# Kernel optimization log

Measured on AMD Instinct MI355X. Metric: run time of the kernel, lower is better.

## Reference

```python
import jax, jax.numpy as jnp
import numpy as np


def setup_inputs() -> dict:
    key = jax.random.key(0)
    k0, k1, k2, k3, k4 = jax.random.split(key, 5)
    dim, b, h, w = 256, 32, 56, 56
    x = jax.random.normal(k0, (b, dim, h, w), jnp.float32)
    # 1x1 conv qk: weight [out=dim, in=dim], bias [dim]
    qk_w = jax.random.normal(k1, (dim, dim), jnp.float32) * (1.0 / np.sqrt(dim))
    qk_b = jax.random.normal(k2, (dim,), jnp.float32) * 0.01
    # depthwise 3x3 conv pe: weight [dim, 1, 3, 3], bias [dim]
    pe_w = jax.random.normal(k3, (dim, 1, 3, 3), jnp.float32) * (1.0 / 3.0)
    pe_b = jax.random.normal(k4, (dim,), jnp.float32) * 0.01
    return {"x": x, "qk_w": qk_w, "qk_b": qk_b, "pe_w": pe_w, "pe_b": pe_b}


def reference(x, qk_w, qk_b, pe_w, pe_b):
    b, c, h, w = x.shape
    n = h * w
    d = c // 2                      # head_dim = dim // 2
    s = float(n) ** -0.5
    # 1x1 conv + (elu + 1) feature map
    qk = jnp.einsum('bchw,oc->bohw', x, qk_w) + qk_b[None, :, None, None]
    qk = jax.nn.elu(qk) + 1.0
    qk = qk.reshape(b, 2, d, n)
    q, k = qk[:, 0], qk[:, 1]       # each [b, d, n]
    v = x.reshape(b, c, n)          # [b, c, n]
    # kv outer product: (k*s) @ (v^T * s) -> [b, d, c]
    kv = jnp.einsum('bdn,bcn->bdc', k, v) * (s * s)
    # numerator q^T @ kv -> [b, n, c]
    num = jnp.einsum('bdn,bdc->bnc', q, kv)
    # denominator q^T @ mean(k, axis=-1) -> [b, n, 1]
    den = jnp.einsum('bdn,bd->bn', q, jnp.mean(k, axis=-1))[:, :, None] + 1e-6
    attn = (num / den).transpose(0, 2, 1).reshape(b, c, h, w)
    # depthwise 3x3 positional conv on v (= x)
    pe = jax.lax.conv_general_dilated(
        x, pe_w, window_strides=(1, 1), padding='SAME',
        dimension_numbers=('NCHW', 'OIHW', 'NCHW'), feature_group_count=c)
    return attn + pe + pe_b[None, :, None, None]
```

## Files before the change

kernel.cpp:

```cpp
#include <hip/hip_runtime.h>

#define B_ 32
#define C_ 256
#define D_ 128
#define HH 56
#define WW 56
#define N_ 3136
#define KSPLIT 14
#define KRANGE 224

typedef float f32x4 __attribute__((ext_vector_type(4)));
typedef short s16x8 __attribute__((ext_vector_type(8)));
typedef unsigned short u16x8 __attribute__((ext_vector_type(8)));

__device__ __forceinline__ int swz4(int r){
  return (r & 3) ^ (((r >> 2) & 1) << 1) ^ ((r >> 3) & 1);
}
__device__ __forceinline__ unsigned short f2bf(float f){
  unsigned u = __float_as_uint(f);
  u += 0x7fffu + ((u >> 16) & 1u);
  return (unsigned short)(u >> 16);
}
__device__ __forceinline__ float bf2f(unsigned short h){
  return __uint_as_float(((unsigned)h) << 16);
}
__device__ __forceinline__ float elu1(float v){
  return v > 0.f ? v + 1.f : __expf(v);
}

template<int R>
__device__ __forceinline__ void stage_glds(const unsigned short* gp, int ld, char* lds){
  const int tid = threadIdx.x;
  const int wid = tid >> 6;
#pragma unroll
  for (int q = 0; q < R/64; ++q){
    const int slot = q*256 + tid;
    const int r = slot >> 2, gi = slot & 3;
    const int u = gi ^ swz4(r);
    const unsigned short* ga = gp + r*ld + u*8;
    char* lb = lds + (q*256 + wid*64)*16;
    __builtin_amdgcn_global_load_lds(
        (__attribute__((address_space(1))) void*)ga,
        (__attribute__((address_space(3))) void*)lb, 16, 0, 0);
  }
}

__device__ __forceinline__ s16x8 ldsfrag(const char* lds, int r, int g){
  return *(const s16x8*)(lds + r*64 + ((g ^ swz4(r)) << 4));
}

__global__ __launch_bounds__(256) void k1_qk(
    const float* __restrict__ x, const float* __restrict__ w,
    const float* __restrict__ bias,
    unsigned short* __restrict__ kbuf, unsigned short* __restrict__ qt)
{
  __shared__ __align__(16) char Al[256*64];
  __shared__ __align__(16) char Bl[64*64];
  const int tid = threadIdx.x, lane = tid & 63, wid = tid >> 6;
  const int n0 = blockIdx.x * 64;
  const int b  = blockIdx.y;
  const float* xb = x + (size_t)b*C_*N_;
  const int wo = wid*64;
  f32x4 acc[4][4] = {};

  for (int k0 = 0; k0 < C_; k0 += 32){
    __syncthreads();
#pragma unroll
    for (int q = 0; q < 8; ++q){
      int idx = q*256 + tid;
      int r = idx >> 3, c4 = (idx & 7)*4;
      float4 v = *(const float4*)(w + (size_t)r*C_ + k0 + c4);
      ushort4 hv = {f2bf(v.x), f2bf(v.y), f2bf(v.z), f2bf(v.w)};
      *(ushort4*)(Al + r*64 + ((c4*2) ^ (swz4(r) << 4))) = hv;
    }
#pragma unroll
    for (int q = 0; q < 2; ++q){
      int idx = q*256 + tid;
      int cc = idx >> 4, nn = (idx & 15)*4;
      float4 v = *(const float4*)(xb + (size_t)(k0 + cc)*N_ + n0 + nn);
      float vv[4] = {v.x, v.y, v.z, v.w};
#pragma unroll
      for (int i = 0; i < 4; ++i){
        int r = nn + i;
        *(unsigned short*)(Bl + r*64 + ((cc*2) ^ (swz4(r) << 4))) = f2bf(vv[i]);
      }
    }
    __syncthreads();
    s16x8 af[4], bv4[4];
#pragma unroll
    for (int m = 0; m < 4; ++m)  af[m]  = ldsfrag(Al, wo + m*16 + (lane & 15), lane >> 4);
#pragma unroll
    for (int nf = 0; nf < 4; ++nf) bv4[nf] = ldsfrag(Bl, nf*16 + (lane & 15), lane >> 4);
#pragma unroll
    for (int m = 0; m < 4; ++m)
#pragma unroll
      for (int nf = 0; nf < 4; ++nf)
        acc[m][nf] = __builtin_amdgcn_mfma_f32_16x16x32_bf16(af[m], bv4[nf], acc[m][nf], 0, 0, 0);
  }

  const int col = lane & 15, rg = lane >> 4;
  if (wid < 2){
#pragma unroll
    for (int m = 0; m < 4; ++m){
      const int db = wo + m*16 + rg*4;
      const float b0 = bias[db], b1 = bias[db+1], b2 = bias[db+2], b3 = bias[db+3];
#pragma unroll
      for (int nf = 0; nf < 4; ++nf){
        const int n = n0 + nf*16 + col;
        f32x4 a = acc[m][nf];
        ushort4 hv = {f2bf(elu1(a[0]+b0)), f2bf(elu1(a[1]+b1)),
                      f2bf(elu1(a[2]+b2)), f2bf(elu1(a[3]+b3))};
        *(ushort4*)(qt + ((size_t)b*N_ + n)*D_ + db) = hv;
      }
    }
  } else {
#pragma unroll
    for (int m = 0; m < 4; ++m)
#pragma unroll
      for (int j = 0; j < 4; ++j){
        const int d = wo - 128 + m*16 + rg*4 + j;
        const float bb = bias[128 + d];
#pragma unroll
        for (int nf = 0; nf < 4; ++nf){
          const int n = n0 + nf*16 + col;
          kbuf[((size_t)b*D_ + d)*N_ + n] = f2bf(elu1(acc[m][nf][j] + bb));
        }
      }
  }
}

__global__ __launch_bounds__(256) void k2_kv(
    const unsigned short* __restrict__ kbuf, const float* __restrict__ x,
    unsigned short* __restrict__ kvp, float* __restrict__ kmp)
{
  __shared__ __align__(16) char Al[128*64];
  __shared__ __align__(16) char Bl[128*64];
  const int tid = threadIdx.x, lane = tid & 63, wid = tid >> 6;
  const int c0 = blockIdx.x * 128;
  const int ks = blockIdx.y;
  const int b  = blockIdx.z;
  const unsigned short* kb = kbuf + (size_t)b*D_*N_ + ks*KRANGE;
  const float* xb = x + ((size_t)b*C_ + c0)*N_ + ks*KRANGE;
  const int wd = (wid >> 1)*64, wc = (wid & 1)*64;
  f32x4 acc[4][4] = {};
  float kms = 0.f;
  const bool do_km = (c0 == 0);

  for (int t = 0; t < KRANGE/32; ++t){
    __syncthreads();
    stage_glds<128>(kb + t*32, N_, Al);
#pragma unroll
    for (int q = 0; q < 4; ++q){
      int idx = q*256 + tid;
      int cc = idx >> 3, n4 = (idx & 7)*4;
      float4 v = *(const float4*)(xb + (size_t)cc*N_ + t*32 + n4);
      ushort4 hv = {f2bf(v.x), f2bf(v.y), f2bf(v.z), f2bf(v.w)};
      *(ushort4*)(Bl + cc*64 + ((n4*2) ^ (swz4(cc) << 4))) = hv;
    }
    __syncthreads();
    s16x8 af[4], bv4[4];
#pragma unroll
    for (int m = 0; m < 4; ++m)  af[m]  = ldsfrag(Al, wd + m*16 + (lane & 15), lane >> 4);
#pragma unroll
    for (int cf = 0; cf < 4; ++cf) bv4[cf] = ldsfrag(Bl, wc + cf*16 + (lane & 15), lane >> 4);
#pragma unroll
    for (int m = 0; m < 4; ++m)
#pragma unroll
      for (int cf = 0; cf < 4; ++cf)
        acc[m][cf] = __builtin_amdgcn_mfma_f32_16x16x32_bf16(af[m], bv4[cf], acc[m][cf], 0, 0, 0);
    if (do_km){
      const int dr = tid >> 1, half = tid & 1;
      const char* base = Al + dr*64;
      const int s = swz4(dr);
      uint4 u0 = *(const uint4*)(base + (((half*2 + 0) ^ s) << 4));
      uint4 u1 = *(const uint4*)(base + (((half*2 + 1) ^ s) << 4));
      const unsigned ua[8] = {u0.x,u0.y,u0.z,u0.w,u1.x,u1.y,u1.z,u1.w};
#pragma unroll
      for (int i = 0; i < 8; ++i){
        kms += bf2f((unsigned short)(ua[i] & 0xffffu));
        kms += bf2f((unsigned short)(ua[i] >> 16));
      }
    }
  }

  if (do_km){
    kms += __shfl_xor(kms, 1);
    if ((tid & 1) == 0) kmp[((size_t)b*KSPLIT + ks)*D_ + (tid >> 1)] = kms;
  }
  const int col = lane & 15, rg = lane >> 4;
#pragma unroll
  for (int m = 0; m < 4; ++m)
#pragma unroll
    for (int j = 0; j < 4; ++j){
      const int d = wd + m*16 + rg*4 + j;
#pragma unroll
      for (int cf = 0; cf < 4; ++cf){
        const int c = c0 + wc + cf*16 + col;
        kvp[(((size_t)b*KSPLIT + ks)*D_ + d)*C_ + c] = f2bf(acc[m][cf][j]);
      }
    }
}

__global__ __launch_bounds__(256) void kr_reduce(
    const unsigned short* __restrict__ kvp, const float* __restrict__ kmp,
    unsigned short* __restrict__ kvt, float* __restrict__ km)
{
  __shared__ float T[64][65];
  const int tid = threadIdx.x;
  const int ct = blockIdx.x, dt = blockIdx.y, b = blockIdx.z;
  const int d0 = dt*64, c0 = ct*64;
  const int r = tid >> 2, cq = (tid & 3)*16;
  float v[16] = {};
  for (int j = 0; j < KSPLIT; ++j){
    const unsigned short* p = kvp + (((size_t)b*KSPLIT + j)*D_ + d0 + r)*C_ + c0 + cq;
#pragma unroll
    for (int i = 0; i < 16; ++i) v[i] += bf2f(p[i]);
  }
  const float sc = 1.0f/(float)N_;
#pragma unroll
  for (int i = 0; i < 16; ++i) T[r][cq + i] = v[i]*sc;
  __syncthreads();
  u16x8 h0, h1;
#pragma unroll
  for (int i = 0; i < 8; ++i) h0[i] = f2bf(T[cq + i][r]);
#pragma unroll
  for (int i = 0; i < 8; ++i) h1[i] = f2bf(T[cq + 8 + i][r]);
  unsigned short* o = kvt + ((size_t)b*C_ + c0 + r)*D_ + d0 + cq;
  *(u16x8*)o = h0;
  *(u16x8*)(o + 8) = h1;
  if (ct == 0 && dt == 0 && tid < D_){
    float s = 0.f;
    for (int j = 0; j < KSPLIT; ++j) s += kmp[((size_t)b*KSPLIT + j)*D_ + tid];
    km[b*D_ + tid] = s*sc;
  }
}

__global__ __launch_bounds__(256) void k3_attn(
    const unsigned short* __restrict__ qt, const unsigned short* __restrict__ kvt,
    const float* __restrict__ km, unsigned short* __restrict__ attn)
{
  __shared__ __align__(16) char SM[128*72*2];
  char* Al = SM;
  char* Bl = SM + 128*64;
  unsigned short* P = (unsigned short*)SM;
  __shared__ float kms[128];
  __shared__ float dens[64];
  const int tid = threadIdx.x, lane = tid & 63, wid = tid >> 6;
  const int n0 = blockIdx.x * 64;
  const int c0 = blockIdx.y * 128;
  const int b  = blockIdx.z;
  if (tid < 128) kms[tid] = km[b*D_ + tid];
  const unsigned short* kvb = kvt + ((size_t)b*C_ + c0)*D_;
  const unsigned short* qtb = qt + ((size_t)b*N_ + n0)*D_;
  const int wc = (wid >> 1)*64, wn = (wid & 1)*32;
  f32x4 acc[4][2] = {};
  float den = 0.f;

  for (int k0 = 0; k0 < D_; k0 += 32){
    __syncthreads();
    stage_glds<128>(kvb + k0, D_, Al);
    stage_glds<64>(qtb + k0, D_, Bl);
    __syncthreads();
    s16x8 af[4], bv4[2];
#pragma unroll
    for (int m = 0; m < 4; ++m)  af[m]  = ldsfrag(Al, wc + m*16 + (lane & 15), lane >> 4);
#pragma unroll
    for (int nf = 0; nf < 2; ++nf) bv4[nf] = ldsfrag(Bl, wn + nf*16 + (lane & 15), lane >> 4);
#pragma unroll
    for (int m = 0; m < 4; ++m)
#pragma unroll
      for (int nf = 0; nf < 2; ++nf)
        acc[m][nf] = __builtin_amdgcn_mfma_f32_16x16x32_bf16(af[m], bv4[nf], acc[m][nf], 0, 0, 0);
    {
      const int nr = tid >> 2, g = tid & 3;
      uint4 u = *(const uint4*)(Bl + nr*64 + ((g ^ swz4(nr)) << 4));
      const float* kp = kms + k0 + g*8;
      const unsigned ua[4] = {u.x, u.y, u.z, u.w};
#pragma unroll
      for (int i = 0; i < 4; ++i){
        den += bf2f((unsigned short)(ua[i] & 0xffffu)) * kp[i*2];
        den += bf2f((unsigned short)(ua[i] >> 16))     * kp[i*2 + 1];
      }
    }
  }
  den += __shfl_xor(den, 1);
  den += __shfl_xor(den, 2);
  if ((tid & 3) == 0) dens[tid >> 2] = den;
  __syncthreads();

  const int col = lane & 15, rg = lane >> 4;
  float rdv[2];
#pragma unroll
  for (int nf = 0; nf < 2; ++nf)
    rdv[nf] = 1.0f / (dens[wn + nf*16 + col] + 1e-6f);
#pragma unroll
  for (int m = 0; m < 4; ++m)
#pragma unroll
    for (int nf = 0; nf < 2; ++nf)
#pragma unroll
      for (int j = 0; j < 4; ++j)
        P[(wc + m*16 + rg*4 + j)*72 + (wn + nf*16 + col)] = f2bf(acc[m][nf][j] * rdv[nf]);
  __syncthreads();

#pragma unroll
  for (int p = 0; p < 4; ++p){
    const int c = (tid >> 3) + p*32, ch = tid & 7;
    u16x8 v = *(const u16x8*)(P + c*72 + ch*8);
    *(u16x8*)(attn + ((size_t)b*C_ + c0 + c)*N_ + n0 + ch*8) = v;
  }
}

__global__ __launch_bounds__(256) void k4_pe(
    const float* __restrict__ x, const unsigned short* __restrict__ attn,
    const float* __restrict__ pw, const float* __restrict__ pb,
    float* __restrict__ out)
{
  __shared__ float xs[N_];
  const int ch = blockIdx.x, b = blockIdx.y;
  const float* xp = x + ((size_t)b*C_ + ch)*N_;
  for (int i = threadIdx.x; i < N_/4; i += 256)
    ((float4*)xs)[i] = ((const float4*)xp)[i];
  const float* wp = pw + ch*9;
  const float w00=wp[0], w01=wp[1], w02=wp[2];
  const float w10=wp[3], w11=wp[4], w12=wp[5];
  const float w20=wp[6], w21=wp[7], w22=wp[8];
  const float bias = pb[ch];
  __syncthreads();
  const unsigned short* ap = attn + ((size_t)b*C_ + ch)*N_;
  float* op = out + ((size_t)b*C_ + ch)*N_;
  for (int i = threadIdx.x; i < N_; i += 256) {
    const int hh = i / WW, ww = i - hh*WW;
    float s = bias;
    if (hh > 0) {
      const float* rp = &xs[(hh-1)*WW];
      if (ww > 0)      s += w00 * rp[ww-1];
                       s += w01 * rp[ww];
      if (ww < WW-1)   s += w02 * rp[ww+1];
    }
    {
      const float* rp = &xs[hh*WW];
      if (ww > 0)      s += w10 * rp[ww-1];
                       s += w11 * rp[ww];
      if (ww < WW-1)   s += w12 * rp[ww+1];
    }
    if (hh < HH-1) {
      const float* rp = &xs[(hh+1)*WW];
      if (ww > 0)      s += w20 * rp[ww-1];
                       s += w21 * rp[ww];
      if (ww < WW-1)   s += w22 * rp[ww+1];
    }
    op[i] = bf2f(ap[i]) + s;
  }
}

extern "C" void kernel_launch(void* const* d_in, const int* in_sizes, int n_in,
                              void* d_out, int out_size, void* d_ws, size_t ws_size,
                              hipStream_t stream) {
  (void)in_sizes; (void)n_in; (void)out_size; (void)ws_size;
  const float* x   = (const float*)d_in[0];
  const float* qkw = (const float*)d_in[1];
  const float* qkb = (const float*)d_in[2];
  const float* pew = (const float*)d_in[3];
  const float* peb = (const float*)d_in[4];
  float* out = (float*)d_out;

  unsigned short* kbuf = (unsigned short*)d_ws;
  unsigned short* qt   = kbuf + (size_t)B_*D_*N_;
  unsigned short* kvt  = qt   + (size_t)B_*N_*D_;
  float* km  = (float*)(kvt + (size_t)B_*C_*D_);
  unsigned short* kvp  = (unsigned short*)(km + (size_t)B_*D_);
  float* kmp = (float*)(kvp + (size_t)B_*KSPLIT*D_*C_);
  unsigned short* attn = kvp;

  k1_qk    <<<dim3(N_/64, B_),         256, 0, stream>>>(x, qkw, qkb, kbuf, qt);
  k2_kv    <<<dim3(C_/128, KSPLIT, B_),256, 0, stream>>>(kbuf, x, kvp, kmp);
  kr_reduce<<<dim3(4, 2, B_),          256, 0, stream>>>(kvp, kmp, kvt, km);
  k3_attn  <<<dim3(N_/64, 2, B_),      256, 0, stream>>>(qt, kvt, km, attn);
  k4_pe    <<<dim3(C_, B_),            256, 0, stream>>>(x, attn, pew, peb, out);
}
```

Before: 181.0 us.

## Pre-transpose x and weights to bf16, use async LDS loads, widen kv tile

Adds pre-pass kernels that convert the qk weight to bf16 and transpose x into an [b,n,c] bf16 layout. k1 can then stage both operands with direct global-to-LDS loads instead of doing per-element conversion and scattered LDS stores. k2 now covers all 256 channels per block, so k is loaded once rather than twice, and the k-sum runs in every block. Hardware packed bf16 conversion replaces the manual rounding in several places. The cost is an extra full pass over x (read fp32, write bf16), more workspace aliasing, and twice the accumulator registers in k2.

New measurement: 186.7 us. +3.1%, slower.

```diff
diff --git a/kernel.cpp b/kernel.cpp
--- a/kernel.cpp
+++ b/kernel.cpp
@@ -26,6 +26,11 @@
 }
 __device__ __forceinline__ float elu1(float v){
   return v > 0.f ? v + 1.f : __expf(v);
+}
+__device__ __forceinline__ unsigned cvtpk(float lo, float hi){
+  unsigned r;
+  asm("v_cvt_pk_bf16_f32 %0, %1, %2" : "=v"(r) : "v"(lo), "v"(hi));
+  return r;
 }
 
 template<int R>
@@ -49,8 +54,41 @@
   return *(const s16x8*)(lds + r*64 + ((g ^ swz4(r)) << 4));
 }
 
+__global__ __launch_bounds__(256) void k0_w(
+    const float* __restrict__ w, unsigned short* __restrict__ wb)
+{
+  const int i = blockIdx.x*256 + threadIdx.x;
+  float4 v = *(const float4*)(w + (size_t)i*4);
+  uint2 h = {cvtpk(v.x, v.y), cvtpk(v.z, v.w)};
+  *(uint2*)(wb + (size_t)i*4) = h;
+}
+
+__global__ __launch_bounds__(256) void k0_t(
+    const float* __restrict__ x, unsigned short* __restrict__ xt)
+{
+  __shared__ float T[64][65];
+  const int tid = threadIdx.x;
+  const int n0 = blockIdx.x*64, c0 = blockIdx.y*64, b = blockIdx.z;
+  const float* xb = x + ((size_t)b*C_ + c0)*N_ + n0;
+#pragma unroll
+  for (int q = 0; q < 4; ++q){
+    const int cr = q*16 + (tid >> 4), nc = (tid & 15)*4;
+    float4 v = *(const float4*)(xb + (size_t)cr*N_ + nc);
+    T[cr][nc+0] = v.x; T[cr][nc+1] = v.y; T[cr][nc+2] = v.z; T[cr][nc+3] = v.w;
+  }
+  __syncthreads();
+  const int nn = tid >> 2, cq = tid & 3;
+  unsigned h[8];
+#pragma unroll
+  for (int j = 0; j < 8; ++j)
+    h[j] = cvtpk(T[cq*16 + 2*j][nn], T[cq*16 + 2*j + 1][nn]);
+  unsigned short* dst = xt + ((size_t)b*N_ + n0 + nn)*C_ + c0 + cq*16;
+  *(uint4*)dst       = (uint4){h[0], h[1], h[2], h[3]};
+  *(uint4*)(dst + 8) = (uint4){h[4], h[5], h[6], h[7]};
+}
+
 __global__ __launch_bounds__(256) void k1_qk(
-    const float* __restrict__ x, const float* __restrict__ w,
+    const unsigned short* __restrict__ xt, const unsigned short* __restrict__ wb,
     const float* __restrict__ bias,
     unsigned short* __restrict__ kbuf, unsigned short* __restrict__ qt)
 {
@@ -59,32 +97,14 @@
   const int tid = threadIdx.x, lane = tid & 63, wid = tid >> 6;
   const int n0 = blockIdx.x * 64;
   const int b  = blockIdx.y;
-  const float* xb = x + (size_t)b*C_*N_;
+  const unsigned short* xtb = xt + ((size_t)b*N_ + n0)*C_;
   const int wo = wid*64;
   f32x4 acc[4][4] = {};
 
   for (int k0 = 0; k0 < C_; k0 += 32){
     __syncthreads();
-#pragma unroll
-    for (int q = 0; q < 8; ++q){
-      int idx = q*256 + tid;
-      int r = idx >> 3, c4 = (idx & 7)*4;
-      float4 v = *(const float4*)(w + (size_t)r*C_ + k0 + c4);
-      ushort4 hv = {f2bf(v.x), f2bf(v.y), f2bf(v.z), f2bf(v.w)};
-      *(ushort4*)(Al + r*64 + ((c4*2) ^ (swz4(r) << 4))) = hv;
-    }
-#pragma unroll
-    for (int q = 0; q < 2; ++q){
-      int idx = q*256 + tid;
-      int cc = idx >> 4, nn = (idx & 15)*4;
-      float4 v = *(const float4*)(xb + (size_t)(k0 + cc)*N_ + n0 + nn);
-      float vv[4] = {v.x, v.y, v.z, v.w};
-#pragma unroll
-      for (int i = 0; i < 4; ++i){
-        int r = nn + i;
-        *(unsigned short*)(Bl + r*64 + ((cc*2) ^ (swz4(r) << 4))) = f2bf(vv[i]);
-      }
-    }
+    stage_glds<256>(wb + k0, C_, Al);
+    stage_glds<64>(xtb + k0, C_, Bl);
     __syncthreads();
     s16x8 af[4], bv4[4];
 #pragma unroll
@@ -108,9 +128,9 @@
       for (int nf = 0; nf < 4; ++nf){
         const int n = n0 + nf*16 + col;
         f32x4 a = acc[m][nf];
-        ushort4 hv = {f2bf(elu1(a[0]+b0)), f2bf(elu1(a[1]+b1)),
-                      f2bf(elu1(a[2]+b2)), f2bf(elu1(a[3]+b3))};
-        *(ushort4*)(qt + ((size_t)b*N_ + n)*D_ + db) = hv;
+        uint2 hv = {cvtpk(elu1(a[0]+b0), elu1(a[1]+b1)),
+                    cvtpk(elu1(a[2]+b2), elu1(a[3]+b3))};
+        *(uint2*)(qt + ((size_t)b*N_ + n)*D_ + db) = hv;
       }
     }
   } else {
@@ -134,41 +154,39 @@
     unsigned short* __restrict__ kvp, float* __restrict__ kmp)
 {
   __shared__ __align__(16) char Al[128*64];
-  __shared__ __align__(16) char Bl[128*64];
+  __shared__ __align__(16) char Bl[256*64];
   const int tid = threadIdx.x, lane = tid & 63, wid = tid >> 6;
-  const int c0 = blockIdx.x * 128;
-  const int ks = blockIdx.y;
-  const int b  = blockIdx.z;
+  const int ks = blockIdx.x;
+  const int b  = blockIdx.y;
   const unsigned short* kb = kbuf + (size_t)b*D_*N_ + ks*KRANGE;
-  const float* xb = x + ((size_t)b*C_ + c0)*N_ + ks*KRANGE;
-  const int wd = (wid >> 1)*64, wc = (wid & 1)*64;
-  f32x4 acc[4][4] = {};
+  const float* xb = x + (size_t)b*C_*N_ + ks*KRANGE;
+  const int wd = (wid >> 1)*64, wc = (wid & 1)*128;
+  f32x4 acc[4][8] = {};
   float kms = 0.f;
-  const bool do_km = (c0 == 0);
 
   for (int t = 0; t < KRANGE/32; ++t){
     __syncthreads();
     stage_glds<128>(kb + t*32, N_, Al);
 #pragma unroll
-    for (int q = 0; q < 4; ++q){
+    for (int q = 0; q < 8; ++q){
       int idx = q*256 + tid;
       int cc = idx >> 3, n4 = (idx & 7)*4;
       float4 v = *(const float4*)(xb + (size_t)cc*N_ + t*32 + n4);
-      ushort4 hv = {f2bf(v.x), f2bf(v.y), f2bf(v.z), f2bf(v.w)};
-      *(ushort4*)(Bl + cc*64 + ((n4*2) ^ (swz4(cc) << 4))) = hv;
-    }
-    __syncthreads();
-    s16x8 af[4], bv4[4];
-#pragma unroll
-    for (int m = 0; m < 4; ++m)  af[m]  = ldsfrag(Al, wd + m*16 + (lane & 15), lane >> 4);
-#pragma unroll
-    for (int cf = 0; cf < 4; ++cf) bv4[cf] = ldsfrag(Bl, wc + cf*16 + (lane & 15), lane >> 4);
+      uint2 h = {cvtpk(v.x, v.y), cvtpk(v.z, v.w)};
+      *(uint2*)(Bl + cc*64 + ((n4*2) ^ (swz4(cc) << 4))) = h;
+    }
+    __syncthreads();
+    s16x8 af[4], bv[8];
+#pragma unroll
+    for (int m = 0; m < 4; ++m)  af[m] = ldsfrag(Al, wd + m*16 + (lane & 15), lane >> 4);
+#pragma unroll
+    for (int cf = 0; cf < 8; ++cf) bv[cf] = ldsfrag(Bl, wc + cf*16 + (lane & 15), lane >> 4);
 #pragma unroll
     for (int m = 0; m < 4; ++m)
 #pragma unroll
-      for (int cf = 0; cf < 4; ++cf)
-        acc[m][cf] = __builtin_amdgcn_mfma_f32_16x16x32_bf16(af[m], bv4[cf], acc[m][cf], 0, 0, 0);
-    if (do_km){
+      for (int cf = 0; cf < 8; ++cf)
+        acc[m][cf] = __builtin_amdgcn_mfma_f32_16x16x32_bf16(af[m], bv[cf], acc[m][cf], 0, 0, 0);
+    {
       const int dr = tid >> 1, half = tid & 1;
       const char* base = Al + dr*64;
       const int s = swz4(dr);
@@ -183,10 +201,9 @@
     }
   }
 
-  if (do_km){
-    kms += __shfl_xor(kms, 1);
-    if ((tid & 1) == 0) kmp[((size_t)b*KSPLIT + ks)*D_ + (tid >> 1)] = kms;
-  }
+  kms += __shfl_xor(kms, 1);
+  if ((tid & 1) == 0) kmp[((size_t)b*KSPLIT + ks)*D_ + (tid >> 1)] = kms;
+
   const int col = lane & 15, rg = lane >> 4;
 #pragma unroll
   for (int m = 0; m < 4; ++m)
@@ -194,8 +211,8 @@
     for (int j = 0; j < 4; ++j){
       const int d = wd + m*16 + rg*4 + j;
 #pragma unroll
-      for (int cf = 0; cf < 4; ++cf){
-        const int c = c0 + wc + cf*16 + col;
+      for (int cf = 0; cf < 8; ++cf){
+        const int c = wc + cf*16 + col;
         kvp[(((size_t)b*KSPLIT + ks)*D_ + d)*C_ + c] = f2bf(acc[m][cf][j]);
       }
     }
@@ -364,17 +381,21 @@
   const float* peb = (const float*)d_in[4];
   float* out = (float*)d_out;
 
-  unsigned short* kbuf = (unsigned short*)d_ws;
+  unsigned short* xts  = (unsigned short*)d_ws;
+  unsigned short* kbuf = xts + (size_t)B_*N_*C_;
   unsigned short* qt   = kbuf + (size_t)B_*D_*N_;
   unsigned short* kvt  = qt   + (size_t)B_*N_*D_;
   float* km  = (float*)(kvt + (size_t)B_*C_*D_);
-  unsigned short* kvp  = (unsigned short*)(km + (size_t)B_*D_);
+  unsigned short* wb   = kvt;
+  unsigned short* kvp  = xts;
   float* kmp = (float*)(kvp + (size_t)B_*KSPLIT*D_*C_);
-  unsigned short* attn = kvp;
-
-  k1_qk    <<<dim3(N_/64, B_),         256, 0, stream>>>(x, qkw, qkb, kbuf, qt);
-  k2_kv    <<<dim3(C_/128, KSPLIT, B_),256, 0, stream>>>(kbuf, x, kvp, kmp);
-  kr_reduce<<<dim3(4, 2, B_),          256, 0, stream>>>(kvp, kmp, kvt, km);
-  k3_attn  <<<dim3(N_/64, 2, B_),      256, 0, stream>>>(qt, kvt, km, attn);
-  k4_pe    <<<dim3(C_, B_),            256, 0, stream>>>(x, attn, pew, peb, out);
-}
+  unsigned short* attn = xts;
+
+  k0_w     <<<dim3(64),                 256, 0, stream>>>(qkw, wb);
+  k0_t     <<<dim3(N_/64, C_/64, B_),   256, 0, stream>>>(x, xts);
+  k1_qk    <<<dim3(N_/64, B_),          256, 0, stream>>>(xts, wb, qkb, kbuf, qt);
+  k2_kv    <<<dim3(KSPLIT, B_),         256, 0, stream>>>(kbuf, x, kvp, kmp);
+  kr_reduce<<<dim3(4, 2, B_),           256, 0, stream>>>(kvp, kmp, kvt, km);
+  k3_attn  <<<dim3(N_/64, 2, B_),       256, 0, stream>>>(qt, kvt, km, attn);
+  k4_pe    <<<dim3(C_, B_),             256, 0, stream>>>(x, attn, pew, peb, out);
+}
```
